# Performance work log

Hardware: AMD Instinct MI355X
Metric: run time of the kernel (lower is better)

The kernel has to match this reference:

```python
import jax, jax.numpy as jnp
import numpy as np

B, C_ATT, C_VAL = 1, 64, 64
T, H, W = 40, 32, 32
HW = H * W
TOPK = 10
TEMP = 0.07
NEIGHBOR_RANGE = 24  # circle mode -> radius = 24 // 2
NON_MASK_LEN = 1     # first frame is not masked
NEG_INF = -1e30


def _spatial_neighbor_circle(h, w, neighbor_range):
    """Circle-mode spatial neighbor mask, (h*w, h*w) bool."""
    radius = neighbor_range // 2
    gy, gx = jnp.meshgrid(jnp.arange(h, dtype=jnp.float32),
                          jnp.arange(w, dtype=jnp.float32), indexing='ij')
    dy = gy[:, :, None, None] - gy[None, None, :, :]
    dx = gx[:, :, None, None] - gx[None, None, :, :]
    dist = jnp.sqrt(dy * dy + dx * dx)
    return (dist < radius).reshape(h * w, h * w)


def setup_inputs() -> dict:
    key0 = jax.random.key(0)
    k1, k2, k3 = jax.random.split(key0, 3)
    query = jax.random.normal(k1, (B, C_ATT, H, W), dtype=jnp.float32)
    key = jax.random.normal(k2, (B, C_ATT, T, H, W), dtype=jnp.float32)
    value = jax.random.normal(k3, (B, C_VAL, T, H, W), dtype=jnp.float32)
    mask = _spatial_neighbor_circle(H, W, NEIGHBOR_RANGE)  # (HW, HW) bool
    return {"query": query, "key": key, "value": value, "mask": mask}


def _l2_normalize(x, axis, eps=1e-12):
    # matches F.normalize(p=2): x / max(||x||, eps)
    n = jnp.sqrt(jnp.sum(x * x, axis=axis, keepdims=True))
    return x / jnp.maximum(n, eps)


def reference(query, key, value, mask):
    # normalize along channel dim
    q = _l2_normalize(query, axis=1).reshape(B, C_ATT, HW)          # (B,C,Q)
    k = _l2_normalize(key, axis=1).reshape(B, C_ATT, T * HW)        # (B,C,K)
    v = value.reshape(B, C_VAL, T * HW)                             # (B,Cv,K)

    # affinity over all keys vs all queries (chunking in the original is a
    # pure memory optimization; the math per query column is identical)
    aff = jnp.einsum('bck,bcq->bkq', k, q) / TEMP                   # (B,K,Q)

    # build full mask: first NON_MASK_LEN frames fully visible, remaining
    # frames restricted to the spatial-neighbor circle
    tiled = jnp.tile(mask, (T - NON_MASK_LEN, 1))                   # ((T-nm)*HW, Q)
    full_mask = jnp.concatenate(
        [jnp.ones((NON_MASK_LEN * HW, HW), dtype=bool), tiled], axis=0)  # (K,Q)
    aff = jnp.where(full_mask[None], aff, NEG_INF)

    # top-k over the key dimension, per query
    aff_qk = jnp.swapaxes(aff, 1, 2)                                # (B,Q,K)
    top_vals, top_idx = jax.lax.top_k(aff_qk, TOPK)                 # (B,Q,topk)
    weights = jax.nn.softmax(top_vals, axis=-1)                     # (B,Q,topk)

    # gather top-k values: (B,Cv,Q,topk)
    gathered = jnp.take_along_axis(v[:, :, None, :], top_idx[:, None, :, :], axis=3)
    out = jnp.einsum('bcqk,bqk->bcq', gathered, weights)            # (B,Cv,Q)
    return out.reshape(B, C_VAL, H, W)
```

## Files before the change

### kernel.cpp

```cpp
#include <hip/hip_runtime.h>
#include <hip/hip_bf16.h>
#include <float.h>

#define HWQ   1024
#define NK    40960
#define NCH   64
#define NTOP  10
#define NJOBS 47
#define NPART (NJOBS * NTOP)
#define R2    144
#define CAP   48
#define TSCALE 14.2857142857142857f
#define LOSCL  4.8828125e-4f

typedef _Float16 f16x8 __attribute__((ext_vector_type(8)));
typedef float    f32x4 __attribute__((ext_vector_type(4)));
typedef unsigned short us8 __attribute__((ext_vector_type(8)));
typedef unsigned long long u64;
typedef unsigned int       u32;

__device__ inline float bf16bits_to_f32(unsigned short u) {
    union { u32 i; float f; } z; z.i = ((u32)u) << 16; return z.f;
}
__device__ inline unsigned short f32_to_bf16bits(float x) {
    __hip_bfloat16 b = __float2bfloat16(x);
    return *(unsigned short*)&b;
}

__device__ inline int sniff_fp32(const unsigned short* __restrict__ raw) {
    const int lane = threadIdx.x & 63;
    const int e = (raw[lane] >> 7) & 0xFF;
    const u64 m = __ballot(e < 100 || e > 133);
    return __popcll(m) > 16;
}

__device__ inline u32 ord32(float v) {
    const u32 b = __float_as_uint(v);
    return b ^ (u32)(((int)b >> 31) | (int)0x80000000);
}
__device__ inline float unpack_ord32(u32 u) {
    const u32 b = u ^ (~((u32)((int)u >> 31)) | 0x80000000u);
    return __uint_as_float(b);
}
__device__ inline u64 pack_vi(float val, int kidx) {
    return ((u64)ord32(val) << 16) | (u32)(0xFFFF - kidx);
}
__device__ inline float unpack_val(u64 p) { return unpack_ord32((u32)(p >> 16)); }
__device__ inline int unpack_idx(u64 p) { return 0xFFFF - (int)(p & 0xFFFF); }

__device__ inline void ins10(u64* v, u64 pk) {
#pragma unroll
    for (int j = NTOP - 1; j >= 1; --j) {
        const bool gj = pk > v[j];
        const bool gp = pk > v[j - 1];
        v[j] = gj ? (gp ? v[j - 1] : pk) : v[j];
    }
    if (pk > v[0]) v[0] = pk;
}

__global__ __launch_bounds__(256) void prep_all(
    const void* __restrict__ qin_, const void* __restrict__ kin_,
    const void* __restrict__ vin_,
    f16x8* __restrict__ kh, f16x8* __restrict__ kl,
    f16x8* __restrict__ qh, f16x8* __restrict__ ql,
    unsigned short* __restrict__ vt, u32* __restrict__ thmax)
{
    const int isf = sniff_fp32((const unsigned short*)kin_);
    const int bid = blockIdx.x;
    const int tid = threadIdx.x;
    const int cg  = tid & 3;
    const int c0  = cg * 16;

    if (bid == 655) {
        ((u32*)thmax)[tid * 4 + 0] = 0; ((u32*)thmax)[tid * 4 + 1] = 0;
        ((u32*)thmax)[tid * 4 + 2] = 0; ((u32*)thmax)[tid * 4 + 3] = 0;
    }

    if (bid < NK / 64) {
        const int key = bid * 64 + (tid >> 2);
        float x[16];
        if (isf) {
            const float* p = (const float*)kin_;
#pragma unroll
            for (int i = 0; i < 16; ++i) x[i] = p[(c0 + i) * NK + key];
        } else {
            const __hip_bfloat16* p = (const __hip_bfloat16*)kin_;
#pragma unroll
            for (int i = 0; i < 16; ++i) x[i] = __bfloat162float(p[(c0 + i) * NK + key]);
        }
        float s = 0.f;
#pragma unroll
        for (int i = 0; i < 16; ++i) s = fmaf(x[i], x[i], s);
        s += __shfl_xor(s, 1); s += __shfl_xor(s, 2);
        const float rn = 1.0f / fmaxf(sqrtf(s), 1e-12f);

        const int tb = (key >> 4) * 128 + (key & 15);
#pragma unroll
        for (int b2 = 0; b2 < 2; ++b2) {
            f16x8 h, l;
#pragma unroll
            for (int jj = 0; jj < 8; ++jj) {
                const float xv = x[b2 * 8 + jj] * rn;
                const _Float16 hh = (_Float16)xv;
                h[jj] = hh;
                l[jj] = (_Float16)((xv - (float)hh) * 2048.0f);
            }
            kh[tb + (cg * 2 + b2) * 16] = h;
            kl[tb + (cg * 2 + b2) * 16] = l;
        }

        unsigned short vv[16];
        if (isf) {
            const float* p = (const float*)vin_;
#pragma unroll
            for (int i = 0; i < 16; ++i) vv[i] = f32_to_bf16bits(p[(c0 + i) * NK + key]);
        } else {
            const unsigned short* p = (const unsigned short*)vin_;
#pragma unroll
            for (int i = 0; i < 16; ++i) vv[i] = p[(c0 + i) * NK + key];
        }
        us8* dst = (us8*)(vt + (size_t)key * NCH + c0);
#pragma unroll
        for (int b2 = 0; b2 < 2; ++b2) {
            us8 o;
#pragma unroll
            for (int e = 0; e < 8; ++e) o[e] = vv[b2 * 8 + e];
            dst[b2] = o;
        }
    } else {
        const int q = (bid - NK / 64) * 64 + (tid >> 2);
        float x[16];
        if (isf) {
            const float* p = (const float*)qin_;
#pragma unroll
            for (int i = 0; i < 16; ++i) x[i] = p[(c0 + i) * HWQ + q];
        } else {
            const __hip_bfloat16* p = (const __hip_bfloat16*)qin_;
#pragma unroll
            for (int i = 0; i < 16; ++i) x[i] = __bfloat162float(p[(c0 + i) * HWQ + q]);
        }
        float s = 0.f;
#pragma unroll
        for (int i = 0; i < 16; ++i) s = fmaf(x[i], x[i], s);
        s += __shfl_xor(s, 1); s += __shfl_xor(s, 2);
        const float rn = 1.0f / fmaxf(sqrtf(s), 1e-12f);

        const int tb = (q >> 4) * 128 + (q & 15);
#pragma unroll
        for (int b2 = 0; b2 < 2; ++b2) {
            f16x8 h, l;
#pragma unroll
            for (int jj = 0; jj < 8; ++jj) {
                const float xv = x[b2 * 8 + jj] * rn;
                const _Float16 hh = (_Float16)xv;
                h[jj] = hh;
                l[jj] = (_Float16)((xv - (float)hh) * 2048.0f);
            }
            qh[tb + (cg * 2 + b2) * 16] = h;
            ql[tb + (cg * 2 + b2) * 16] = l;
        }
    }
}

__device__ inline void quad_merge_store(
    u64 (*sm)[16][NTOP], int lane, u64* out10)
{
    int p0 = 0, p1 = 0, p2 = 0, p3 = 0;
#pragma unroll
    for (int r = 0; r < NTOP; ++r) {
        const u64 h0 = sm[0][lane][p0], h1 = sm[1][lane][p1];
        const u64 h2 = sm[2][lane][p2], h3 = sm[3][lane][p3];
        u64 m = h0; int sel = 0;
        if (h1 > m) { m = h1; sel = 1; }
        if (h2 > m) { m = h2; sel = 2; }
        if (h3 > m) { m = h3; sel = 3; }
        out10[r] = m;
        p0 += (sel == 0); p1 += (sel == 1); p2 += (sel == 2); p3 += (sel == 3);
    }
}

__global__ __launch_bounds__(128) void attn_f0(
    const f16x8* __restrict__ kh, const f16x8* __restrict__ kl,
    const f16x8* __restrict__ qh, const f16x8* __restrict__ ql,
    u64* __restrict__ pv, u32* __restrict__ thmax)
{
    __shared__ u64 sm[2][4][16][NTOP];

    const int tid  = threadIdx.x;
    const int w    = tid >> 6;
    const int lane = tid & 63;
    const int quad = lane >> 4;
    const int n    = lane & 15;

    const int t   = blockIdx.x * 2 + w;
    const int job = blockIdx.y;

    const int qb = t * 128 + n;
    const f16x8 bh0 = qh[qb + quad * 16];
    const f16x8 bh1 = qh[qb + (4 + quad) * 16];
    const f16x8 bl0 = ql[qb + quad * 16];
    const f16x8 bl1 = ql[qb + (4 + quad) * 16];

    u64 v[NTOP];
#pragma unroll
    for (int jj = 0; jj < NTOP; ++jj) v[jj] = 0ull;

    const int start = job * 8, end = start + 8;
    const int loff = (n + quad * 16) * 16;
    const char* ph = (const char*)kh + (size_t)start * 2048 + loff;
    const char* pl = (const char*)kl + (size_t)start * 2048 + loff;

    f16x8 Ah0 = *(const f16x8*)(ph);
    f16x8 Ah1 = *(const f16x8*)(ph + 1024);
    f16x8 Al0 = *(const f16x8*)(pl);
    f16x8 Al1 = *(const f16x8*)(pl + 1024);

    for (int kt = start; kt < end; ++kt) {
        const size_t adv = (kt + 1 < end) ? 2048 : 0;
        const char* nh = ph + adv;
        const char* nl = pl + adv;
        const f16x8 Bh0 = *(const f16x8*)(nh);
        const f16x8 Bh1 = *(const f16x8*)(nh + 1024);
        const f16x8 Bl0 = *(const f16x8*)(nl);
        const f16x8 Bl1 = *(const f16x8*)(nl + 1024);

        f32x4 accH = {0.f,0.f,0.f,0.f}, accL0 = {0.f,0.f,0.f,0.f}, accL1 = {0.f,0.f,0.f,0.f};
        accH  = __builtin_amdgcn_mfma_f32_16x16x32_f16(Ah0, bh0, accH, 0, 0, 0);
        accH  = __builtin_amdgcn_mfma_f32_16x16x32_f16(Ah1, bh1, accH, 0, 0, 0);
        accL0 = __builtin_amdgcn_mfma_f32_16x16x32_f16(Ah0, bl0, accL0, 0, 0, 0);
        accL0 = __builtin_amdgcn_mfma_f32_16x16x32_f16(Al0, bh0, accL0, 0, 0, 0);
        accL1 = __builtin_amdgcn_mfma_f32_16x16x32_f16(Ah1, bl1, accL1, 0, 0, 0);
        accL1 = __builtin_amdgcn_mfma_f32_16x16x32_f16(Al1, bh1, accL1, 0, 0, 0);

        const int key0 = kt * 16 + quad * 4;
#pragma unroll
        for (int r = 0; r < 4; ++r) {
            const float val = fmaf(accL0[r] + accL1[r], LOSCL, accH[r]);
            const u64 pk = pack_vi(val, key0 + r);
            if (pk > v[NTOP - 1]) ins10(v, pk);
        }
        Ah0 = Bh0; Ah1 = Bh1; Al0 = Bl0; Al1 = Bl1;
        ph = nh; pl = nl;
    }

#pragma unroll
    for (int jj = 0; jj < NTOP; ++jj) sm[w][quad][n][jj] = v[jj];
    __syncthreads();

    if (lane < 16) {
        u64 out10[NTOP];
        quad_merge_store(sm[w], lane, out10);
        const int q = t * 16 + lane;
#pragma unroll
        for (int r = 0; r < NTOP; ++r) pv[(size_t)q * NPART + job * NTOP + r] = out10[r];
        atomicMax(&thmax[q], (u32)(out10[9] >> 16));
    }
}

__global__ __launch_bounds__(128) void attn_masked(
    const f16x8* __restrict__ kh, const f16x8* __restrict__ kl,
    const f16x8* __restrict__ qh, const f16x8* __restrict__ ql,
    const u32* __restrict__ thmax, u64* __restrict__ pv)
{
    __shared__ u64 cand[32][CAP];
    __shared__ int cnt[32];

    const int tid  = threadIdx.x;
    const int w    = tid >> 6;
    const int lane = tid & 63;
    const int quad = lane >> 4;
    const int n    = lane & 15;

    const int lin   = blockIdx.x;
    const int j     = (lin & 7) * 156 + (lin >> 3);
    const int fm1   = j >> 5;
    const int qy    = j & 31;
    const int frame = fm1 + 1;

    if (tid < 32) cnt[tid] = 0;
    __syncthreads();

    const int q0 = qy * 32 + n;
    const float theta0 = unpack_ord32(thmax[q0]);
    const float theta1 = unpack_ord32(thmax[q0 + 16]);

    const int qb = (qy * 2) * 128 + n;
    const f16x8 b0h0 = qh[qb + quad * 16];
    const f16x8 b0h1 = qh[qb + (4 + quad) * 16];
    const f16x8 b0l0 = ql[qb + quad * 16];
    const f16x8 b0l1 = ql[qb + (4 + quad) * 16];
    const f16x8 b1h0 = qh[qb + 128 + quad * 16];
    const f16x8 b1h1 = qh[qb + 128 + (4 + quad) * 16];
    const f16x8 b1l0 = ql[qb + 128 + quad * 16];
    const f16x8 b1l1 = ql[qb + 128 + (4 + quad) * 16];

    const int rlo = (qy > 11) ? qy - 11 : 0;
    const int rhi = (qy < 20) ? qy + 11 : 31;
    const int mid = (rlo + rhi + 1) >> 1;
    const int r0  = w ? mid : rlo;
    const int r1  = w ? (rhi + 1) : mid;

    const int loff = (n + quad * 16) * 16;
    const char* ph = (const char*)kh + (size_t)(frame * 64 + 2 * r0) * 2048 + loff;
    const char* pl = (const char*)kl + (size_t)(frame * 64 + 2 * r0) * 2048 + loff;

    f16x8 Ahe0 = *(const f16x8*)(ph);
    f16x8 Ahe1 = *(const f16x8*)(ph + 1024);
    f16x8 Aho0 = *(const f16x8*)(ph + 2048);
    f16x8 Aho1 = *(const f16x8*)(ph + 3072);
    f16x8 Ale0 = *(const f16x8*)(pl);
    f16x8 Ale1 = *(const f16x8*)(pl + 1024);
    f16x8 Alo0 = *(const f16x8*)(pl + 2048);
    f16x8 Alo1 = *(const f16x8*)(pl + 3072);

    for (int row = r0; row < r1; ++row) {
        const size_t adv = (row + 1 < r1) ? 4096 : 0;
        const char* nh = ph + adv;
        const char* nl = pl + adv;
        const f16x8 Bhe0 = *(const f16x8*)(nh);
        const f16x8 Bhe1 = *(const f16x8*)(nh + 1024);
        const f16x8 Bho0 = *(const f16x8*)(nh + 2048);
        const f16x8 Bho1 = *(const f16x8*)(nh + 3072);
        const f16x8 Ble0 = *(const f16x8*)(nl);
        const f16x8 Ble1 = *(const f16x8*)(nl + 1024);
        const f16x8 Blo0 = *(const f16x8*)(nl + 2048);
        const f16x8 Blo1 = *(const f16x8*)(nl + 3072);

        const int dy = row - qy;
        const int rem = R2 - dy * dy;
        const int keyrow = frame * 1024 + row * 32;

#pragma unroll
        for (int p = 0; p < 2; ++p) {
            const f16x8 ah0 = p ? Aho0 : Ahe0;
            const f16x8 ah1 = p ? Aho1 : Ahe1;
            const f16x8 al0 = p ? Alo0 : Ale0;
            const f16x8 al1 = p ? Alo1 : Ale1;

            f32x4 aH0 = {0.f,0.f,0.f,0.f}, aL00 = {0.f,0.f,0.f,0.f}, aL01 = {0.f,0.f,0.f,0.f};
            f32x4 aH1 = {0.f,0.f,0.f,0.f}, aL10 = {0.f,0.f,0.f,0.f}, aL11 = {0.f,0.f,0.f,0.f};
            aH0  = __builtin_amdgcn_mfma_f32_16x16x32_f16(ah0, b0h0, aH0, 0, 0, 0);
            aH0  = __builtin_amdgcn_mfma_f32_16x16x32_f16(ah1, b0h1, aH0, 0, 0, 0);
            aL00 = __builtin_amdgcn_mfma_f32_16x16x32_f16(ah0, b0l0, aL00, 0, 0, 0);
            aL00 = __builtin_amdgcn_mfma_f32_16x16x32_f16(al0, b0h0, aL00, 0, 0, 0);
            aL01 = __builtin_amdgcn_mfma_f32_16x16x32_f16(ah1, b0l1, aL01, 0, 0, 0);
            aL01 = __builtin_amdgcn_mfma_f32_16x16x32_f16(al1, b0h1, aL01, 0, 0, 0);
            aH1  = __builtin_amdgcn_mfma_f32_16x16x32_f16(ah0, b1h0, aH1, 0, 0, 0);
            aH1  = __builtin_amdgcn_mfma_f32_16x16x32_f16(ah1, b1h1, aH1, 0, 0, 0);
            aL10 = __builtin_amdgcn_mfma_f32_16x16x32_f16(ah0, b1l0, aL10, 0, 0, 0);
            aL10 = __builtin_amdgcn_mfma_f32_16x16x32_f16(al0, b1h0, aL10, 0, 0, 0);
            aL11 = __builtin_amdgcn_mfma_f32_16x16x32_f16(ah1, b1l1, aL11, 0, 0, 0);
            aL11 = __builtin_amdgcn_mfma_f32_16x16x32_f16(al1, b1h1, aL11, 0, 0, 0);

            const int kx0 = p * 16 + quad * 4;
            const int key0 = keyrow + kx0;
#pragma unroll
            for (int r = 0; r < 4; ++r) {
                const float v0 = fmaf(aL00[r] + aL01[r], LOSCL, aH0[r]);
                const float v1 = fmaf(aL10[r] + aL11[r], LOSCL, aH1[r]);
                const int dx0 = kx0 + r - n;
                const int dx1 = dx0 - 16;
                if (v0 > theta0 && dx0 * dx0 < rem) {
                    const int pos = atomicAdd(&cnt[n], 1);
                    if (pos < CAP) cand[n][pos] = pack_vi(v0, key0 + r);
                }
                if (v1 > theta1 && dx1 * dx1 < rem) {
                    const int pos = atomicAdd(&cnt[16 + n], 1);
                    if (pos < CAP) cand[16 + n][pos] = pack_vi(v1, key0 + r);
                }
            }
        }
        Ahe0 = Bhe0; Ahe1 = Bhe1; Aho0 = Bho0; Aho1 = Bho1;
        Ale0 = Ble0; Ale1 = Ble1; Alo0 = Blo0; Alo1 = Blo1;
        ph = nh; pl = nl;
    }

    __syncthreads();
    if (tid < 32) {
        const int c = min(cnt[tid], CAP);
        u64 v[NTOP];
#pragma unroll
        for (int e = 0; e < NTOP; ++e) v[e] = 0ull;
        for (int e = 0; e < c; ++e) {
            const u64 pk = cand[tid][e];
            if (pk > v[NTOP - 1]) ins10(v, pk);
        }
        const int qq  = qy * 32 + tid;
        const int job = 8 + fm1;
#pragma unroll
        for (int r = 0; r < NTOP; ++r)
            pv[(size_t)qq * NPART + (size_t)job * NTOP + r] = v[r];
    }
}

__global__ __launch_bounds__(64) void finalize_kernel(
    const u64* __restrict__ pv, const unsigned short* __restrict__ vt,
    const unsigned short* __restrict__ kin_raw, void* __restrict__ out_)
{
    const int isf  = sniff_fp32(kin_raw);
    const int q    = blockIdx.x;
    const int lane = threadIdx.x;

    u64 lv[8];
#pragma unroll
    for (int e = 0; e < 8; ++e) {
        const int idx = e * 64 + lane;
        lv[e] = (idx < NPART) ? pv[(size_t)q * NPART + idx] : 0ull;
    }

    float wv[NTOP]; int wi[NTOP];
#pragma unroll
    for (int r = 0; r < NTOP; ++r) {
        u64 m = lv[0];
#pragma unroll
        for (int e = 1; e < 8; ++e) if (lv[e] > m) m = lv[e];
#pragma unroll
        for (int off = 32; off >= 1; off >>= 1) {
            const u32 lo = (u32)m, hi = (u32)(m >> 32);
            const u32 lo2 = (u32)__shfl_xor((int)lo, off);
            const u32 hi2 = (u32)__shfl_xor((int)hi, off);
            const u64 o = ((u64)hi2 << 32) | lo2;
            if (o > m) m = o;
        }
#pragma unroll
        for (int e = 0; e < 8; ++e) if (lv[e] == m) lv[e] = 0ull;
        wv[r] = unpack_val(m); wi[r] = unpack_idx(m);
    }

    float ww[NTOP]; float wsum = 0.f;
#pragma unroll
    for (int r = 0; r < NTOP; ++r) { ww[r] = expf((wv[r] - wv[0]) * TSCALE); wsum += ww[r]; }
    const float inv = 1.0f / wsum;

    float acc = 0.f;
#pragma unroll
    for (int r = 0; r < NTOP; ++r)
        acc += ww[r] * bf16bits_to_f32(vt[(size_t)wi[r] * NCH + lane]);
    const float res = acc * inv;

    if (isf) ((float*)out_)[lane * HWQ + q] = res;
    else     ((__hip_bfloat16*)out_)[lane * HWQ + q] = __float2bfloat16(res);
}

extern "C" void kernel_launch(void* const* d_in, const int* in_sizes, int n_in,
                              void* d_out, int out_size, void* d_ws, size_t ws_size,
                              hipStream_t stream)
{
    const void* qin = d_in[0];
    const void* kin = d_in[1];
    const void* vin = d_in[2];

    char* w = (char*)d_ws;
    f16x8*          kh    = (f16x8*)(w);
    f16x8*          kl    = (f16x8*)(w + 5242880);
    f16x8*          qhv   = (f16x8*)(w + 10485760);
    f16x8*          qlv   = (f16x8*)(w + 10616832);
    unsigned short* vt    = (unsigned short*)(w + 10747904);
    u64*            pv    = (u64*)(w + 15990784);
    u32*            thmax = (u32*)(w + 19841024);

    prep_all<<<656, 256, 0, stream>>>(qin, kin, vin, kh, kl, qhv, qlv, vt, thmax);
    attn_f0<<<dim3(32, 8), 128, 0, stream>>>(kh, kl, qhv, qlv, pv, thmax);
    attn_masked<<<1248, 128, 0, stream>>>(kh, kl, qhv, qlv, thmax, pv);
    finalize_kernel<<<HWQ, 64, 0, stream>>>(pv, vt, (const unsigned short*)kin, d_out);
}
```

Measured before the change: 135.5 us.

## Use exact frame-0 top-10 threshold and global candidate lists with balanced masked work

Adds a theta_refine kernel that computes each query's exact 10th-best frame-0 score and uses it as the pruning threshold, instead of the max over per-job 10th bests. The masked pass becomes 4096 single-wave blocks that split a flat list of circle-valid (frame, query-row, key-row) units evenly. Survivors are appended to per-query global candidate buffers via global atomics, and finalize merges them directly with the 80 frame-0 partials. Prep now reduces channel norms across waves through shared memory, and the register prefetch in attn_f0 is removed. This removes the per-frame partial writes and the imbalanced row ranges, but adds a kernel launch, global atomics, and a risk of overflowing the fixed 384-entry candidate capacity.

```diff
diff --git a/kernel.cpp b/kernel.cpp
--- a/kernel.cpp
+++ b/kernel.cpp
@@ -6,10 +6,12 @@
 #define NK    40960
 #define NCH   64
 #define NTOP  10
-#define NJOBS 47
-#define NPART (NJOBS * NTOP)
+#define NF0JOB 8
+#define PVLEN (NF0JOB * NTOP)
+#define CAPG  384
 #define R2    144
-#define CAP   48
+#define TOTU  23556
+#define NBLK  4096
 #define TSCALE 14.2857142857142857f
 #define LOSCL  4.8828125e-4f
 
@@ -38,14 +40,14 @@
     const u32 b = __float_as_uint(v);
     return b ^ (u32)(((int)b >> 31) | (int)0x80000000);
 }
-__device__ inline float unpack_ord32(u32 u) {
+__device__ inline u64 pack_vi(float val, int kidx) {
+    return ((u64)ord32(val) << 16) | (u32)(0xFFFF - kidx);
+}
+__device__ inline float unpack_val(u64 p) {
+    const u32 u = (u32)(p >> 16);
     const u32 b = u ^ (~((u32)((int)u >> 31)) | 0x80000000u);
     return __uint_as_float(b);
 }
-__device__ inline u64 pack_vi(float val, int kidx) {
-    return ((u64)ord32(val) << 16) | (u32)(0xFFFF - kidx);
-}
-__device__ inline float unpack_val(u64 p) { return unpack_ord32((u32)(p >> 16)); }
 __device__ inline int unpack_idx(u64 p) { return 0xFFFF - (int)(p & 0xFFFF); }
 
 __device__ inline void ins10(u64* v, u64 pk) {
@@ -63,21 +65,23 @@
     const void* __restrict__ vin_,
     f16x8* __restrict__ kh, f16x8* __restrict__ kl,
     f16x8* __restrict__ qh, f16x8* __restrict__ ql,
-    unsigned short* __restrict__ vt, u32* __restrict__ thmax)
-{
-    const int isf = sniff_fp32((const unsigned short*)kin_);
-    const int bid = blockIdx.x;
-    const int tid = threadIdx.x;
-    const int cg  = tid & 3;
-    const int c0  = cg * 16;
+    unsigned short* __restrict__ vt, int* __restrict__ cnt)
+{
+    __shared__ float ssq[4][64];
+    const int isf  = sniff_fp32((const unsigned short*)kin_);
+    const int bid  = blockIdx.x;
+    const int tid  = threadIdx.x;
+    const int w    = tid >> 6;
+    const int lane = tid & 63;
+    const int c0   = w * 16;
 
     if (bid == 655) {
-        ((u32*)thmax)[tid * 4 + 0] = 0; ((u32*)thmax)[tid * 4 + 1] = 0;
-        ((u32*)thmax)[tid * 4 + 2] = 0; ((u32*)thmax)[tid * 4 + 3] = 0;
-    }
-
-    if (bid < NK / 64) {
-        const int key = bid * 64 + (tid >> 2);
+        cnt[tid * 4 + 0] = 0; cnt[tid * 4 + 1] = 0;
+        cnt[tid * 4 + 2] = 0; cnt[tid * 4 + 3] = 0;
+    }
+
+    if (bid < 640) {
+        const int key = bid * 64 + lane;
         float x[16];
         if (isf) {
             const float* p = (const float*)kin_;
@@ -91,7 +95,9 @@
         float s = 0.f;
 #pragma unroll
         for (int i = 0; i < 16; ++i) s = fmaf(x[i], x[i], s);
-        s += __shfl_xor(s, 1); s += __shfl_xor(s, 2);
+        ssq[w][lane] = s;
+        __syncthreads();
+        s = ssq[0][lane] + ssq[1][lane] + ssq[2][lane] + ssq[3][lane];
         const float rn = 1.0f / fmaxf(sqrtf(s), 1e-12f);
 
         const int tb = (key >> 4) * 128 + (key & 15);
@@ -105,8 +111,8 @@
                 h[jj] = hh;
                 l[jj] = (_Float16)((xv - (float)hh) * 2048.0f);
             }
-            kh[tb + (cg * 2 + b2) * 16] = h;
-            kl[tb + (cg * 2 + b2) * 16] = l;
+            kh[tb + (w * 2 + b2) * 16] = h;
+            kl[tb + (w * 2 + b2) * 16] = l;
         }
 
         unsigned short vv[16];
@@ -128,7 +134,7 @@
             dst[b2] = o;
         }
     } else {
-        const int q = (bid - NK / 64) * 64 + (tid >> 2);
+        const int q = (bid - 640) * 64 + lane;
         float x[16];
         if (isf) {
             const float* p = (const float*)qin_;
@@ -142,7 +148,9 @@
         float s = 0.f;
 #pragma unroll
         for (int i = 0; i < 16; ++i) s = fmaf(x[i], x[i], s);
-        s += __shfl_xor(s, 1); s += __shfl_xor(s, 2);
+        ssq[w][lane] = s;
+        __syncthreads();
+        s = ssq[0][lane] + ssq[1][lane] + ssq[2][lane] + ssq[3][lane];
         const float rn = 1.0f / fmaxf(sqrtf(s), 1e-12f);
 
         const int tb = (q >> 4) * 128 + (q & 15);
@@ -156,8 +164,8 @@
                 h[jj] = hh;
                 l[jj] = (_Float16)((xv - (float)hh) * 2048.0f);
             }
-            qh[tb + (cg * 2 + b2) * 16] = h;
-            ql[tb + (cg * 2 + b2) * 16] = l;
+            qh[tb + (w * 2 + b2) * 16] = h;
+            ql[tb + (w * 2 + b2) * 16] = l;
         }
     }
 }
@@ -182,7 +190,7 @@
 __global__ __launch_bounds__(128) void attn_f0(
     const f16x8* __restrict__ kh, const f16x8* __restrict__ kl,
     const f16x8* __restrict__ qh, const f16x8* __restrict__ ql,
-    u64* __restrict__ pv, u32* __restrict__ thmax)
+    u64* __restrict__ pv)
 {
     __shared__ u64 sm[2][4][16][NTOP];
 
@@ -210,19 +218,11 @@
     const char* ph = (const char*)kh + (size_t)start * 2048 + loff;
     const char* pl = (const char*)kl + (size_t)start * 2048 + loff;
 
-    f16x8 Ah0 = *(const f16x8*)(ph);
-    f16x8 Ah1 = *(const f16x8*)(ph + 1024);
-    f16x8 Al0 = *(const f16x8*)(pl);
-    f16x8 Al1 = *(const f16x8*)(pl + 1024);
-
     for (int kt = start; kt < end; ++kt) {
-        const size_t adv = (kt + 1 < end) ? 2048 : 0;
-        const char* nh = ph + adv;
-        const char* nl = pl + adv;
-        const f16x8 Bh0 = *(const f16x8*)(nh);
-        const f16x8 Bh1 = *(const f16x8*)(nh + 1024);
-        const f16x8 Bl0 = *(const f16x8*)(nl);
-        const f16x8 Bl1 = *(const f16x8*)(nl + 1024);
+        const f16x8 Ah0 = *(const f16x8*)(ph);
+        const f16x8 Ah1 = *(const f16x8*)(ph + 1024);
+        const f16x8 Al0 = *(const f16x8*)(pl);
+        const f16x8 Al1 = *(const f16x8*)(pl + 1024);
 
         f32x4 accH = {0.f,0.f,0.f,0.f}, accL0 = {0.f,0.f,0.f,0.f}, accL1 = {0.f,0.f,0.f,0.f};
         accH  = __builtin_amdgcn_mfma_f32_16x16x32_f16(Ah0, bh0, accH, 0, 0, 0);
@@ -239,8 +239,7 @@
             const u64 pk = pack_vi(val, key0 + r);
             if (pk > v[NTOP - 1]) ins10(v, pk);
         }
-        Ah0 = Bh0; Ah1 = Bh1; Al0 = Bl0; Al1 = Bl1;
-        ph = nh; pl = nl;
+        ph += 2048; pl += 2048;
     }
 
 #pragma unroll
@@ -252,149 +251,148 @@
         quad_merge_store(sm[w], lane, out10);
         const int q = t * 16 + lane;
 #pragma unroll
-        for (int r = 0; r < NTOP; ++r) pv[(size_t)q * NPART + job * NTOP + r] = out10[r];
-        atomicMax(&thmax[q], (u32)(out10[9] >> 16));
-    }
-}
-
-__global__ __launch_bounds__(128) void attn_masked(
+        for (int r = 0; r < NTOP; ++r) pv[(size_t)q * PVLEN + job * NTOP + r] = out10[r];
+    }
+}
+
+__global__ __launch_bounds__(256) void theta_refine(
+    const u64* __restrict__ pv, float* __restrict__ thmax)
+{
+    const int q    = blockIdx.x * 4 + (threadIdx.x >> 6);
+    const int lane = threadIdx.x & 63;
+
+    u64 l0 = pv[(size_t)q * PVLEN + lane];
+    u64 l1 = (lane < 16) ? pv[(size_t)q * PVLEN + 64 + lane] : 0ull;
+
+    u64 m = 0ull;
+#pragma unroll
+    for (int r = 0; r < NTOP; ++r) {
+        u64 c = l0 > l1 ? l0 : l1;
+#pragma unroll
+        for (int off = 32; off >= 1; off >>= 1) {
+            const u32 lo = (u32)c, hi = (u32)(c >> 32);
+            const u32 lo2 = (u32)__shfl_xor((int)lo, off);
+            const u32 hi2 = (u32)__shfl_xor((int)hi, off);
+            const u64 o = ((u64)hi2 << 32) | lo2;
+            if (o > c) c = o;
+        }
+        if (l0 == c) l0 = 0ull;
+        if (l1 == c) l1 = 0ull;
+        m = c;
+    }
+    if (lane == 0) thmax[q] = unpack_val(m);
+}
+
+__global__ __launch_bounds__(64) void attn_masked(
     const f16x8* __restrict__ kh, const f16x8* __restrict__ kl,
     const f16x8* __restrict__ qh, const f16x8* __restrict__ ql,
-    const u32* __restrict__ thmax, u64* __restrict__ pv)
-{
-    __shared__ u64 cand[32][CAP];
-    __shared__ int cnt[32];
-
-    const int tid  = threadIdx.x;
-    const int w    = tid >> 6;
-    const int lane = tid & 63;
+    const float* __restrict__ thmax,
+    u64* __restrict__ gcand, int* __restrict__ cnt)
+{
+    const int lane = threadIdx.x;
     const int quad = lane >> 4;
     const int n    = lane & 15;
 
-    const int lin   = blockIdx.x;
-    const int j     = (lin & 7) * 156 + (lin >> 3);
-    const int fm1   = j >> 5;
-    const int qy    = j & 31;
-    const int frame = fm1 + 1;
-
-    if (tid < 32) cnt[tid] = 0;
-    __syncthreads();
-
-    const int q0 = qy * 32 + n;
-    const float theta0 = unpack_ord32(thmax[q0]);
-    const float theta1 = unpack_ord32(thmax[q0 + 16]);
-
-    const int qb = (qy * 2) * 128 + n;
-    const f16x8 b0h0 = qh[qb + quad * 16];
-    const f16x8 b0h1 = qh[qb + (4 + quad) * 16];
-    const f16x8 b0l0 = ql[qb + quad * 16];
-    const f16x8 b0l1 = ql[qb + (4 + quad) * 16];
-    const f16x8 b1h0 = qh[qb + 128 + quad * 16];
-    const f16x8 b1h1 = qh[qb + 128 + (4 + quad) * 16];
-    const f16x8 b1l0 = ql[qb + 128 + quad * 16];
-    const f16x8 b1l1 = ql[qb + 128 + (4 + quad) * 16];
-
-    const int rlo = (qy > 11) ? qy - 11 : 0;
-    const int rhi = (qy < 20) ? qy + 11 : 31;
-    const int mid = (rlo + rhi + 1) >> 1;
-    const int r0  = w ? mid : rlo;
-    const int r1  = w ? (rhi + 1) : mid;
-
-    const int loff = (n + quad * 16) * 16;
-    const char* ph = (const char*)kh + (size_t)(frame * 64 + 2 * r0) * 2048 + loff;
-    const char* pl = (const char*)kl + (size_t)(frame * 64 + 2 * r0) * 2048 + loff;
-
-    f16x8 Ahe0 = *(const f16x8*)(ph);
-    f16x8 Ahe1 = *(const f16x8*)(ph + 1024);
-    f16x8 Aho0 = *(const f16x8*)(ph + 2048);
-    f16x8 Aho1 = *(const f16x8*)(ph + 3072);
-    f16x8 Ale0 = *(const f16x8*)(pl);
-    f16x8 Ale1 = *(const f16x8*)(pl + 1024);
-    f16x8 Alo0 = *(const f16x8*)(pl + 2048);
-    f16x8 Alo1 = *(const f16x8*)(pl + 3072);
-
-    for (int row = r0; row < r1; ++row) {
-        const size_t adv = (row + 1 < r1) ? 4096 : 0;
-        const char* nh = ph + adv;
-        const char* nl = pl + adv;
-        const f16x8 Bhe0 = *(const f16x8*)(nh);
-        const f16x8 Bhe1 = *(const f16x8*)(nh + 1024);
-        const f16x8 Bho0 = *(const f16x8*)(nh + 2048);
-        const f16x8 Bho1 = *(const f16x8*)(nh + 3072);
-        const f16x8 Ble0 = *(const f16x8*)(nl);
-        const f16x8 Ble1 = *(const f16x8*)(nl + 1024);
-        const f16x8 Blo0 = *(const f16x8*)(nl + 2048);
-        const f16x8 Blo1 = *(const f16x8*)(nl + 3072);
-
-        const int dy = row - qy;
-        const int rem = R2 - dy * dy;
+    const int wid = (blockIdx.x & 7) * (NBLK / 8) + (blockIdx.x >> 3);
+    const int u0  = (int)(((long long)wid * TOTU) >> 12);
+    const int u1  = (int)(((long long)(wid + 1) * TOTU) >> 12);
+
+    f16x8 b0h0, b0h1, b0l0, b0l1, b1h0, b1h1, b1l0, b1l1;
+    float theta0 = 0.f, theta1 = 0.f;
+    int cur_qy = -1, q0 = 0;
+
+    for (int u = u0; u < u1; ++u) {
+        const int fm1 = u / 604;
+        const int rem = u - fm1 * 604;
+        int qy, off;
+        if (rem < 210) {
+            int t = (int)((sqrtf((float)(529 + 8 * rem)) - 23.0f) * 0.5f);
+            while ((t * (t + 23)) / 2 > rem) --t;
+            while (((t + 1) * (t + 24)) / 2 <= rem) ++t;
+            qy = t; off = rem - (t * (t + 23)) / 2;
+        } else if (rem < 417) {
+            qy = 12 + (rem - 210) / 23; off = (rem - 210) % 23;
+        } else {
+            const int s = 603 - rem;
+            int t = (int)((sqrtf((float)(529 + 8 * s)) - 23.0f) * 0.5f);
+            while ((t * (t + 23)) / 2 > s) --t;
+            while (((t + 1) * (t + 24)) / 2 <= s) ++t;
+            qy = 31 - t;
+            off = (12 + t) - 1 - (s - (t * (t + 23)) / 2);
+        }
+        const int rlo = (qy > 11) ? qy - 11 : 0;
+        const int row = rlo + off;
+        const int frame = fm1 + 1;
+
+        if (qy != cur_qy) {
+            cur_qy = qy;
+            const int qb = qy * 256 + n;
+            b0h0 = qh[qb + quad * 16];       b0h1 = qh[qb + (4 + quad) * 16];
+            b0l0 = ql[qb + quad * 16];       b0l1 = ql[qb + (4 + quad) * 16];
+            b1h0 = qh[qb + 128 + quad * 16]; b1h1 = qh[qb + 128 + (4 + quad) * 16];
+            b1l0 = ql[qb + 128 + quad * 16]; b1l1 = ql[qb + 128 + (4 + quad) * 16];
+            q0 = qy * 32 + n;
+            theta0 = thmax[q0];
+            theta1 = thmax[q0 + 16];
+        }
+
+        const int dy   = row - qy;
+        const int rem2 = R2 - dy * dy;
+        const int tbase = frame * 64 + row * 2;
         const int keyrow = frame * 1024 + row * 32;
 
-#pragma unroll
-        for (int p = 0; p < 2; ++p) {
-            const f16x8 ah0 = p ? Aho0 : Ahe0;
-            const f16x8 ah1 = p ? Aho1 : Ahe1;
-            const f16x8 al0 = p ? Alo0 : Ale0;
-            const f16x8 al1 = p ? Alo1 : Ale1;
-
-            f32x4 aH0 = {0.f,0.f,0.f,0.f}, aL00 = {0.f,0.f,0.f,0.f}, aL01 = {0.f,0.f,0.f,0.f};
-            f32x4 aH1 = {0.f,0.f,0.f,0.f}, aL10 = {0.f,0.f,0.f,0.f}, aL11 = {0.f,0.f,0.f,0.f};
-            aH0  = __builtin_amdgcn_mfma_f32_16x16x32_f16(ah0, b0h0, aH0, 0, 0, 0);
-            aH0  = __builtin_amdgcn_mfma_f32_16x16x32_f16(ah1, b0h1, aH0, 0, 0, 0);
-            aL00 = __builtin_amdgcn_mfma_f32_16x16x32_f16(ah0, b0l0, aL00, 0, 0, 0);
-            aL00 = __builtin_amdgcn_mfma_f32_16x16x32_f16(al0, b0h0, aL00, 0, 0, 0);
-            aL01 = __builtin_amdgcn_mfma_f32_16x16x32_f16(ah1, b0l1, aL01, 0, 0, 0);
-            aL01 = __builtin_amdgcn_mfma_f32_16x16x32_f16(al1, b0h1, aL01, 0, 0, 0);
-            aH1  = __builtin_amdgcn_mfma_f32_16x16x32_f16(ah0, b1h0, aH1, 0, 0, 0);
-            aH1  = __builtin_amdgcn_mfma_f32_16x16x32_f16(ah1, b1h1, aH1, 0, 0, 0);
-            aL10 = __builtin_amdgcn_mfma_f32_16x16x32_f16(ah0, b1l0, aL10, 0, 0, 0);
-            aL10 = __builtin_amdgcn_mfma_f32_16x16x32_f16(al0, b1h0, aL10, 0, 0, 0);
-            aL11 = __builtin_amdgcn_mfma_f32_16x16x32_f16(ah1, b1l1, aL11, 0, 0, 0);
-            aL11 = __builtin_amdgcn_mfma_f32_16x16x32_f16(al1, b1h1, aL11, 0, 0, 0);
-
-            const int kx0 = p * 16 + quad * 4;
+#pragma unroll 1
+        for (int kt2 = 0; kt2 < 2; ++kt2) {
+            const f16x8* pA = kh + (tbase + kt2) * 128 + n;
+            const f16x8* pL = kl + (tbase + kt2) * 128 + n;
+            const f16x8 ah0 = pA[quad * 16];
+            const f16x8 ah1 = pA[(4 + quad) * 16];
+            const f16x8 al0 = pL[quad * 16];
+            const f16x8 al1 = pL[(4 + quad) * 16];
+
+            f32x4 H0 = {0.f,0.f,0.f,0.f}, L00 = {0.f,0.f,0.f,0.f}, L01 = {0.f,0.f,0.f,0.f};
+            f32x4 H1 = {0.f,0.f,0.f,0.f}, L10 = {0.f,0.f,0.f,0.f}, L11 = {0.f,0.f,0.f,0.f};
+            H0  = __builtin_amdgcn_mfma_f32_16x16x32_f16(ah0, b0h0, H0, 0, 0, 0);
+            H0  = __builtin_amdgcn_mfma_f32_16x16x32_f16(ah1, b0h1, H0, 0, 0, 0);
+            L00 = __builtin_amdgcn_mfma_f32_16x16x32_f16(ah0, b0l0, L00, 0, 0, 0);
+            L00 = __builtin_amdgcn_mfma_f32_16x16x32_f16(al0, b0h0, L00, 0, 0, 0);
+            L01 = __builtin_amdgcn_mfma_f32_16x16x32_f16(ah1, b0l1, L01, 0, 0, 0);
+            L01 = __builtin_amdgcn_mfma_f32_16x16x32_f16(al1, b0h1, L01, 0, 0, 0);
+            H1  = __builtin_amdgcn_mfma_f32_16x16x32_f16(ah0, b1h0, H1, 0, 0, 0);
+            H1  = __builtin_amdgcn_mfma_f32_16x16x32_f16(ah1, b1h1, H1, 0, 0, 0);
+            L10 = __builtin_amdgcn_mfma_f32_16x16x32_f16(ah0, b1l0, L10, 0, 0, 0);
+            L10 = __builtin_amdgcn_mfma_f32_16x16x32_f16(al0, b1h0, L10, 0, 0, 0);
+            L11 = __builtin_amdgcn_mfma_f32_16x16x32_f16(ah1, b1l1, L11, 0, 0, 0);
+            L11 = __builtin_amdgcn_mfma_f32_16x16x32_f16(al1, b1h1, L11, 0, 0, 0);
+
+            const int kx0  = kt2 * 16 + quad * 4;
             const int key0 = keyrow + kx0;
 #pragma unroll
             for (int r = 0; r < 4; ++r) {
-                const float v0 = fmaf(aL00[r] + aL01[r], LOSCL, aH0[r]);
-                const float v1 = fmaf(aL10[r] + aL11[r], LOSCL, aH1[r]);
-                const int dx0 = kx0 + r - n;
-                const int dx1 = dx0 - 16;
-                if (v0 > theta0 && dx0 * dx0 < rem) {
-                    const int pos = atomicAdd(&cnt[n], 1);
-                    if (pos < CAP) cand[n][pos] = pack_vi(v0, key0 + r);
+                const float v0 = fmaf(L00[r] + L01[r], LOSCL, H0[r]);
+                const float v1 = fmaf(L10[r] + L11[r], LOSCL, H1[r]);
+                if (v0 > theta0) {
+                    const int dx = kx0 + r - n;
+                    if (dx * dx < rem2) {
+                        const int pos = atomicAdd(&cnt[q0], 1);
+                        if (pos < CAPG) gcand[(size_t)q0 * CAPG + pos] = pack_vi(v0, key0 + r);
+                    }
                 }
-                if (v1 > theta1 && dx1 * dx1 < rem) {
-                    const int pos = atomicAdd(&cnt[16 + n], 1);
-                    if (pos < CAP) cand[16 + n][pos] = pack_vi(v1, key0 + r);
+                if (v1 > theta1) {
+                    const int dx = kx0 + r - 16 - n;
+                    if (dx * dx < rem2) {
+                        const int pos = atomicAdd(&cnt[q0 + 16], 1);
+                        if (pos < CAPG) gcand[(size_t)(q0 + 16) * CAPG + pos] = pack_vi(v1, key0 + r);
+                    }
                 }
             }
         }
-        Ahe0 = Bhe0; Ahe1 = Bhe1; Aho0 = Bho0; Aho1 = Bho1;
-        Ale0 = Ble0; Ale1 = Ble1; Alo0 = Blo0; Alo1 = Blo1;
-        ph = nh; pl = nl;
-    }
-
-    __syncthreads();
-    if (tid < 32) {
-        const int c = min(cnt[tid], CAP);
-        u64 v[NTOP];
-#pragma unroll
-        for (int e = 0; e < NTOP; ++e) v[e] = 0ull;
-        for (int e = 0; e < c; ++e) {
-            const u64 pk = cand[tid][e];
-            if (pk > v[NTOP - 1]) ins10(v, pk);
-        }
-        const int qq  = qy * 32 + tid;
-        const int job = 8 + fm1;
-#pragma unroll
-        for (int r = 0; r < NTOP; ++r)
-            pv[(size_t)qq * NPART + (size_t)job * NTOP + r] = v[r];
     }
 }
 
 __global__ __launch_bounds__(64) void finalize_kernel(
-    const u64* __restrict__ pv, const unsigned short* __restrict__ vt,
+    const u64* __restrict__ pv, const u64* __restrict__ gcand,
+    const int* __restrict__ cnt, const unsigned short* __restrict__ vt,
     const unsigned short* __restrict__ kin_raw, void* __restrict__ out_)
 {
     const int isf  = sniff_fp32(kin_raw);
@@ -402,10 +400,13 @@
     const int lane = threadIdx.x;
 
     u64 lv[8];
-#pragma unroll
-    for (int e = 0; e < 8; ++e) {
+    lv[0] = pv[(size_t)q * PVLEN + lane];
+    lv[1] = (lane < 16) ? pv[(size_t)q * PVLEN + 64 + lane] : 0ull;
+    const int c = min(cnt[q], CAPG);
+#pragma unroll
+    for (int e = 0; e < 6; ++e) {
         const int idx = e * 64 + lane;
-        lv[e] = (idx < NPART) ? pv[(size_t)q * NPART + idx] : 0ull;
+        lv[2 + e] = (idx < c) ? gcand[(size_t)q * CAPG + idx] : 0ull;
     }
 
     float wv[NTOP]; int wi[NTOP];
@@ -457,10 +458,14 @@
     f16x8*          qlv   = (f16x8*)(w + 10616832);
     unsigned short* vt    = (unsigned short*)(w + 10747904);
     u64*            pv    = (u64*)(w + 15990784);
-    u32*            thmax = (u32*)(w + 19841024);
-
-    prep_all<<<656, 256, 0, stream>>>(qin, kin, vin, kh, kl, qhv, qlv, vt, thmax);
-    attn_f0<<<dim3(32, 8), 128, 0, stream>>>(kh, kl, qhv, qlv, pv, thmax);
-    attn_masked<<<1248, 128, 0, stream>>>(kh, kl, qhv, qlv, thmax, pv);
-    finalize_kernel<<<HWQ, 64, 0, stream>>>(pv, vt, (const unsigned short*)kin, d_out);
-}
+    u64*            gcand = (u64*)(w + 16646144);
+    float*          thmax = (float*)(w + 19791872);
+    int*            cnt   = (int*)(w + 19795968);
+
+    prep_all<<<656, 256, 0, stream>>>(qin, kin, vin, kh, kl, qhv, qlv, vt, cnt);
+    attn_f0<<<dim3(32, 8), 128, 0, stream>>>(kh, kl, qhv, qlv, pv);
+    theta_refine<<<256, 256, 0, stream>>>(pv, thmax);
+    attn_masked<<<NBLK, 64, 0, stream>>>(kh, kl, qhv, qlv, thmax, gcand, cnt);
+    finalize_kernel<<<HWQ, 64, 0, stream>>>(pv, gcand, cnt, vt,
+                                            (const unsigned short*)kin, d_out);
+}
```

After: 146.7 us. 8.2% more time.
